# Kernel tuning notes

Measured on AMD Instinct MI355X. Metric: run time of the kernel, lower is better.

## Reference

```python
import jax, jax.numpy as jnp
import numpy as np

STATE_DIM = 128
FEATURES = 768
DT_MIN, DT_MAX = 0.001, 0.1


def setup_inputs() -> dict:
    key = jax.random.key(0)
    ks = jax.random.split(key, 8)
    B, S, F, N = 8, 4096, FEATURES, STATE_DIM
    n = jnp.arange(N, dtype=jnp.float32)
    # HiPPO-diag inits (deterministic)
    log_A_real = jnp.log(n + 0.5)
    A_imag = jnp.pi * n
    # lecun_normal: std = 1/sqrt(fan_in), fan_in = axis -2
    B_re = jax.random.normal(ks[0], (N, F), jnp.float32) / jnp.sqrt(N)
    B_im = jax.random.normal(ks[1], (N, F), jnp.float32) / jnp.sqrt(N)
    C_re = jax.random.normal(ks[2], (F, N), jnp.float32) / jnp.sqrt(F)
    C_im = jax.random.normal(ks[3], (F, N), jnp.float32) / jnp.sqrt(F)
    D = jax.random.normal(ks[4], (F,), jnp.float32)
    log_dt = jax.random.uniform(ks[5], (N,), jnp.float32,
                                minval=jnp.log(DT_MIN), maxval=jnp.log(DT_MAX))
    u = jax.random.normal(ks[6], (B, S, F), jnp.float32)
    return {"u": u, "log_A_real": log_A_real, "A_imag": A_imag,
            "B_re": B_re, "B_im": B_im, "C_re": C_re, "C_im": C_im,
            "D": D, "log_dt": log_dt}


def reference(u, log_A_real, A_imag, B_re, B_im, C_re, C_im, D, log_dt):
    B, S, F = u.shape
    N = log_A_real.shape[0]
    dt = jnp.exp(log_dt)                           # [N]
    A_diag = -jnp.exp(log_A_real) + 1j * A_imag    # [N] complex
    A_bar = jnp.exp(A_diag * dt)                   # [N] discretized A
    B_complex = B_re + 1j * B_im                   # [N, F]
    B_bar = (A_bar[:, None] - 1.0) / (A_diag[:, None] + 1e-08) * B_complex
    C_complex = C_re + 1j * C_im                   # [F, N]

    u_f = u.astype(jnp.float32)
    Bu = jnp.einsum('bsf,nf->bsn', u_f, B_bar)     # [B, S, N] complex
    A_exp = jnp.broadcast_to(A_bar[None, None, :], (B, S, N))

    def binary_operator(e1, e2):
        a1, b1 = e1
        a2, b2 = e2
        return (a1 * a2, a2 * b1 + b2)

    _, x_states = jax.lax.associative_scan(binary_operator, (A_exp, Bu), axis=1)
    y = jnp.einsum('fn,bsn->bsf', C_complex, x_states).real
    y = y + D[None, None, :] * u_f
    return y.astype(u.dtype)
```

## Files before the change

### kernel.cpp

```cpp
#include <hip/hip_runtime.h>
#include <hip/hip_bf16.h>
#include <math.h>

typedef __attribute__((ext_vector_type(8))) short short8;
typedef __attribute__((ext_vector_type(4))) float f32x4;
typedef __attribute__((ext_vector_type(4))) unsigned int uint4v;

constexpr int kF = 768;
constexpr int kN = 128;
constexpr int kB = 8;
constexpr int kS = 4096;
constexpr int kM = kB * kS;
constexpr int kChunks = 128;
constexpr int kClen = 32;

constexpr size_t kOffBw      = 4096;
constexpr size_t kOffCw      = 397312;
constexpr size_t kOffFinals  = 790528;
constexpr size_t kOffCarries = 1052672;
constexpr size_t kOffXbf     = 1314816;

__device__ __forceinline__ unsigned short f2bf(float f) {
    unsigned int u = __builtin_bit_cast(unsigned int, f);
    u += 0x7fffu + ((u >> 16) & 1u);
    return (unsigned short)(u >> 16);
}

#define LGKM0_BAR() do { \
    asm volatile("s_waitcnt lgkmcnt(0)" ::: "memory"); \
    __builtin_amdgcn_s_barrier(); \
    __builtin_amdgcn_sched_barrier(0); \
} while (0)

__global__ __launch_bounds__(128)
void pre1(const float* __restrict__ log_A_real, const float* __restrict__ A_imag,
          const float* __restrict__ log_dt, float* __restrict__ ws) {
    int n = threadIdx.x;
    float dt = expf(log_dt[n]);
    float ar = -expf(log_A_real[n]);
    float ai = A_imag[n];
    float er = expf(ar * dt);
    float Ar = er * cosf(ai * dt);
    float Ai = er * sinf(ai * dt);
    float dr = ar + 1e-8f, di = ai;
    float inv = 1.0f / (dr * dr + di * di);
    float nr = Ar - 1.0f, ni = Ai;
    float cr = (nr * dr + ni * di) * inv;
    float ci = (ni * dr - nr * di) * inv;
    float pr = 1.f, pi = 0.f;
    for (int i = 0; i < kClen; ++i) {
        float t = pr * Ar - pi * Ai;
        pi = pr * Ai + pi * Ar;
        pr = t;
    }
    ws[n] = Ar;        ws[128 + n] = Ai;
    ws[256 + n] = pr;  ws[384 + n] = pi;
    ws[512 + n] = cr;  ws[640 + n] = ci;
}

__global__ __launch_bounds__(256)
void pre2(const float* __restrict__ B_re, const float* __restrict__ B_im,
          const float* __restrict__ wsf, unsigned short* __restrict__ bw) {
    int id = blockIdx.x * 256 + threadIdx.x;
    int c = id / kF;
    int f = id - c * kF;
    int n = c & 127;
    float cr = wsf[512 + n], ci = wsf[640 + n];
    float br = B_re[n * kF + f], bi = B_im[n * kF + f];
    float v = (c < 128) ? (cr * br - ci * bi) : (cr * bi + ci * br);
    bw[id] = f2bf(v);
}

__global__ __launch_bounds__(256)
void pre3(const float* __restrict__ C_re, const float* __restrict__ C_im,
          unsigned short* __restrict__ cw) {
    int id = blockIdx.x * 256 + threadIdx.x;
    int f = id >> 8;
    int k = id & 255;
    float v = (k < 128) ? C_re[f * kN + k] : -C_im[f * kN + (k - 128)];
    cw[id] = f2bf(v);
}

__global__ __launch_bounds__(256, 2)
void gemm1(const float* __restrict__ A,
           const unsigned short* __restrict__ W,
           float* __restrict__ Cout) {
    constexpr int K = kF, KT = K / 32;
    __shared__ __align__(16) short As0[128 * 40];
    __shared__ __align__(16) short As1[128 * 40];
    __shared__ __align__(16) short Ws0[128 * 40];
    __shared__ __align__(16) short Ws1[128 * 40];

    const int gx = gridDim.x;
    const int nwg = gx * gridDim.y;
    const int orig = blockIdx.y * gx + blockIdx.x;
    const int cpx = nwg >> 3;
    const int sw = (orig & 7) * cpx + (orig >> 3);
    const int m0 = (sw / gx) * 128;
    const int n0 = (sw % gx) * 128;

    const int t = threadIdx.x;
    const int sr = t >> 1, sh = t & 1;

    const int wave = t >> 6, lane = t & 63;
    const int wr = wave >> 1, wc = wave & 1;
    const int lr = lane & 15, lg = lane >> 4;

    f32x4 acc[4][4] = {};

    f32x4 aA0, aA1, aA2, aA3, aB0, aB1, aB2, aB3;
    uint4v wA0, wA1, wB0, wB1;
    const float* aptr = A + (size_t)(m0 + sr) * K + sh * 16;
    const unsigned short* wptr = W + (size_t)(n0 + sr) * K + sh * 16;

#define G1_LOAD(SET, kt) do { \
    const float* p_ = aptr + (kt) * 32; \
    a##SET##0 = *(const f32x4*)p_;        a##SET##1 = *(const f32x4*)(p_ + 4); \
    a##SET##2 = *(const f32x4*)(p_ + 8);  a##SET##3 = *(const f32x4*)(p_ + 12); \
    const unsigned short* q_ = wptr + (kt) * 32; \
    w##SET##0 = *(const uint4v*)q_; w##SET##1 = *(const uint4v*)(q_ + 8); \
} while (0)

#define G1_WRITE(Asb, Wsb, a0, a1, a2, a3, w0, w1) do { \
    short h_[16]; \
    _Pragma("unroll") for (int e_ = 0; e_ < 4; ++e_) { \
        h_[e_]      = (short)f2bf(a0[e_]); \
        h_[4 + e_]  = (short)f2bf(a1[e_]); \
        h_[8 + e_]  = (short)f2bf(a2[e_]); \
        h_[12 + e_] = (short)f2bf(a3[e_]); \
    } \
    const int o_ = sr * 40 + sh * 16; \
    *(short8*)(&Asb[o_])     = *(short8*)&h_[0]; \
    *(short8*)(&Asb[o_ + 8]) = *(short8*)&h_[8]; \
    *(short8*)(&Wsb[o_])     = *(short8*)&w0; \
    *(short8*)(&Wsb[o_ + 8]) = *(short8*)&w1; \
} while (0)

#define G1_MMA(Asb, Wsb) do { \
    short8 ah_[4], bh_[4]; \
    _Pragma("unroll") for (int i_ = 0; i_ < 4; ++i_) { \
        ah_[i_] = *(const short8*)(&Asb[(wr * 64 + i_ * 16 + lr) * 40 + lg * 8]); \
        bh_[i_] = *(const short8*)(&Wsb[(wc * 64 + i_ * 16 + lr) * 40 + lg * 8]); \
    } \
    _Pragma("unroll") for (int i_ = 0; i_ < 4; ++i_) \
    _Pragma("unroll") for (int j_ = 0; j_ < 4; ++j_) \
        acc[i_][j_] = __builtin_amdgcn_mfma_f32_16x16x32_bf16(ah_[i_], bh_[j_], acc[i_][j_], 0, 0, 0); \
} while (0)

    G1_LOAD(A, 0);
    G1_LOAD(B, 1);
    for (int kt = 0; kt < KT; kt += 2) {
        G1_WRITE(As0, Ws0, aA0, aA1, aA2, aA3, wA0, wA1);
        if (kt + 2 < KT) G1_LOAD(A, kt + 2);
        LGKM0_BAR();
        G1_MMA(As0, Ws0);
        G1_WRITE(As1, Ws1, aB0, aB1, aB2, aB3, wB0, wB1);
        if (kt + 3 < KT) G1_LOAD(B, kt + 3);
        LGKM0_BAR();
        G1_MMA(As1, Ws1);
    }

#pragma unroll
    for (int i = 0; i < 4; ++i)
#pragma unroll
        for (int j = 0; j < 4; ++j) {
            const int col = n0 + wc * 64 + j * 16 + lr;
#pragma unroll
            for (int q = 0; q < 4; ++q) {
                const int row = m0 + wr * 64 + i * 16 + lg * 4 + q;
                Cout[(size_t)row * 256 + col] = acc[i][j][q];
            }
        }
#undef G1_LOAD
#undef G1_WRITE
#undef G1_MMA
}

__global__ __launch_bounds__(128)
void scanA(const float* __restrict__ Bu, const float* __restrict__ wsc,
           float* __restrict__ finals) {
    int n = threadIdx.x;
    int blk = blockIdx.x;
    int b = blk >> 7, c = blk & 127;
    float Ar = wsc[n], Ai = wsc[128 + n];
    float xr = 0.f, xi = 0.f;
    size_t base = ((size_t)(b * kS + c * kClen)) * 256;
#pragma unroll 8
    for (int s = 0; s < kClen; ++s) {
        float br = Bu[base + n], bi = Bu[base + 128 + n];
        float tr = Ar * xr - Ai * xi + br;
        xi = Ar * xi + Ai * xr + bi;
        xr = tr;
        base += 256;
    }
    finals[(size_t)blk * 256 + n] = xr;
    finals[(size_t)blk * 256 + 128 + n] = xi;
}

__global__ __launch_bounds__(128)
void scanB(const float* __restrict__ finals, const float* __restrict__ ws,
           float* __restrict__ carries) {
    int n = threadIdx.x;
    int b = blockIdx.x;
    float Pr = ws[256 + n], Pi = ws[384 + n];
    float xr = 0.f, xi = 0.f;
#pragma unroll 8
    for (int c = 0; c < kChunks; ++c) {
        size_t o = ((size_t)(b * kChunks + c)) * 256;
        carries[o + n] = xr;
        carries[o + 128 + n] = xi;
        float fr = finals[o + n], fi = finals[o + 128 + n];
        float tr = Pr * xr - Pi * xi + fr;
        xi = Pr * xi + Pi * xr + fi;
        xr = tr;
    }
}

__global__ __launch_bounds__(128)
void scanC(const float* __restrict__ Bu, const float* __restrict__ wsc,
           const float* __restrict__ carries, unsigned short* __restrict__ xbf) {
    int n = threadIdx.x;
    int blk = blockIdx.x;
    int b = blk >> 7, c = blk & 127;
    float Ar = wsc[n], Ai = wsc[128 + n];
    size_t co = (size_t)blk * 256;
    float xr = carries[co + n], xi = carries[co + 128 + n];
    size_t base = ((size_t)(b * kS + c * kClen)) * 256;
#pragma unroll 4
    for (int s = 0; s < kClen; ++s) {
        float br = Bu[base + n], bi = Bu[base + 128 + n];
        float tr = Ar * xr - Ai * xi + br;
        xi = Ar * xi + Ai * xr + bi;
        xr = tr;
        xbf[base + n]       = f2bf(xr);
        xbf[base + 128 + n] = f2bf(xi);
        base += 256;
    }
}

__global__ __launch_bounds__(256, 3)
void gemm2(const unsigned short* __restrict__ A,
           const unsigned short* __restrict__ W,
           float* __restrict__ Cout,
           const float* __restrict__ Dp, const float* __restrict__ Up) {
    constexpr int K = 256, KT = 8, Nc = kF;
    __shared__ __align__(16) short As0[128 * 40];
    __shared__ __align__(16) short As1[128 * 40];
    __shared__ __align__(16) short Ws0[128 * 40];
    __shared__ __align__(16) short Ws1[128 * 40];

    const int gx = gridDim.x;
    const int nwg = gx * gridDim.y;
    const int orig = blockIdx.y * gx + blockIdx.x;
    const int cpx = nwg >> 3;
    const int sw = (orig & 7) * cpx + (orig >> 3);
    const int m0 = (sw / gx) * 128;
    const int n0 = (sw % gx) * 128;

    const int t = threadIdx.x;
    const int sr = t >> 1, sh = t & 1;

    const int wave = t >> 6, lane = t & 63;
    const int wr = wave >> 1, wc = wave & 1;
    const int lr = lane & 15, lg = lane >> 4;

    f32x4 acc[4][4] = {};

    uint4v aA0, aA1, aB0, aB1;
    uint4v wA0, wA1, wB0, wB1;
    const unsigned short* aptr = A + (size_t)(m0 + sr) * K + sh * 16;
    const unsigned short* wptr = W + (size_t)(n0 + sr) * K + sh * 16;

#define G2_LOAD(SET, kt) do { \
    const unsigned short* p_ = aptr + (kt) * 32; \
    a##SET##0 = *(const uint4v*)p_; a##SET##1 = *(const uint4v*)(p_ + 8); \
    const unsigned short* q_ = wptr + (kt) * 32; \
    w##SET##0 = *(const uint4v*)q_; w##SET##1 = *(const uint4v*)(q_ + 8); \
} while (0)

#define G2_WRITE(Asb, Wsb, a0, a1, w0, w1) do { \
    const int o_ = sr * 40 + sh * 16; \
    *(short8*)(&Asb[o_])     = *(short8*)&a0; \
    *(short8*)(&Asb[o_ + 8]) = *(short8*)&a1; \
    *(short8*)(&Wsb[o_])     = *(short8*)&w0; \
    *(short8*)(&Wsb[o_ + 8]) = *(short8*)&w1; \
} while (0)

#define G2_MMA(Asb, Wsb) do { \
    short8 ah_[4], bh_[4]; \
    _Pragma("unroll") for (int i_ = 0; i_ < 4; ++i_) { \
        ah_[i_] = *(const short8*)(&Asb[(wr * 64 + i_ * 16 + lr) * 40 + lg * 8]); \
        bh_[i_] = *(const short8*)(&Wsb[(wc * 64 + i_ * 16 + lr) * 40 + lg * 8]); \
    } \
    _Pragma("unroll") for (int i_ = 0; i_ < 4; ++i_) \
    _Pragma("unroll") for (int j_ = 0; j_ < 4; ++j_) \
        acc[i_][j_] = __builtin_amdgcn_mfma_f32_16x16x32_bf16(ah_[i_], bh_[j_], acc[i_][j_], 0, 0, 0); \
} while (0)

    G2_LOAD(A, 0);
    G2_LOAD(B, 1);
    for (int kt = 0; kt < KT; kt += 2) {
        G2_WRITE(As0, Ws0, aA0, aA1, wA0, wA1);
        if (kt + 2 < KT) G2_LOAD(A, kt + 2);
        LGKM0_BAR();
        G2_MMA(As0, Ws0);
        G2_WRITE(As1, Ws1, aB0, aB1, wB0, wB1);
        if (kt + 3 < KT) G2_LOAD(B, kt + 3);
        LGKM0_BAR();
        G2_MMA(As1, Ws1);
    }

#pragma unroll
    for (int i = 0; i < 4; ++i)
#pragma unroll
        for (int j = 0; j < 4; ++j) {
            const int col = n0 + wc * 64 + j * 16 + lr;
#pragma unroll
            for (int q = 0; q < 4; ++q) {
                const int row = m0 + wr * 64 + i * 16 + lg * 4 + q;
                float v = acc[i][j][q];
                v = fmaf(Dp[col], Up[(size_t)row * Nc + col], v);
                Cout[(size_t)row * Nc + col] = v;
            }
        }
#undef G2_LOAD
#undef G2_WRITE
#undef G2_MMA
}

extern "C" void kernel_launch(void* const* d_in, const int* in_sizes, int n_in,
                              void* d_out, int out_size, void* d_ws, size_t ws_size,
                              hipStream_t stream) {
    const float* u          = (const float*)d_in[0];
    const float* log_A_real = (const float*)d_in[1];
    const float* A_imag     = (const float*)d_in[2];
    const float* B_re       = (const float*)d_in[3];
    const float* B_im       = (const float*)d_in[4];
    const float* C_re       = (const float*)d_in[5];
    const float* C_im       = (const float*)d_in[6];
    const float* D          = (const float*)d_in[7];
    const float* log_dt     = (const float*)d_in[8];

    char* wsb = (char*)d_ws;
    float* wsf            = (float*)wsb;
    unsigned short* bw    = (unsigned short*)(wsb + kOffBw);
    unsigned short* cw    = (unsigned short*)(wsb + kOffCw);
    float* finals         = (float*)(wsb + kOffFinals);
    float* carries        = (float*)(wsb + kOffCarries);
    unsigned short* xbf   = (unsigned short*)(wsb + kOffXbf);
    float* y              = (float*)d_out;
    float* Bu             = (float*)d_out;

    pre1<<<1, 128, 0, stream>>>(log_A_real, A_imag, log_dt, wsf);
    pre2<<<(256 * kF) / 256, 256, 0, stream>>>(B_re, B_im, wsf, bw);
    pre3<<<(kF * 256) / 256, 256, 0, stream>>>(C_re, C_im, cw);

    gemm1<<<dim3(2, kM / 128), 256, 0, stream>>>(u, bw, Bu);

    scanA<<<kB * kChunks, 128, 0, stream>>>(Bu, wsf, finals);
    scanB<<<kB, 128, 0, stream>>>(finals, wsf, carries);
    scanC<<<kB * kChunks, 128, 0, stream>>>(Bu, wsf, carries, xbf);

    gemm2<<<dim3(kF / 128, kM / 128), 256, 0, stream>>>(xbf, cw, y, D, u);
}
```

Before: 102.2 us.

## Shrink gemm1 M-tile to 64, triple-buffer register prefetch, raise occupancy

gemm1 now computes 64x128 output tiles instead of 128x128. This halves the per-thread accumulators and A staging registers and doubles the number of workgroups. Global loads move to a three-set register prefetch rotation, with a six-step unrolled loop over the 24 K-tiles. Launch bounds rise to 4 waves per SIMD for both gemm1 and gemm2, aiming at better latency hiding and more parallelism. The cost is lower data reuse per tile, so each W tile is loaded twice as often, and gemm2 may spill registers under the tighter bound.

Result: slower. 127.4 us (+24.6%).

```diff
diff --git a/kernel.cpp b/kernel.cpp
--- a/kernel.cpp
+++ b/kernel.cpp
@@ -81,13 +81,13 @@
     cw[id] = f2bf(v);
 }
 
-__global__ __launch_bounds__(256, 2)
+__global__ __launch_bounds__(256, 4)
 void gemm1(const float* __restrict__ A,
            const unsigned short* __restrict__ W,
            float* __restrict__ Cout) {
     constexpr int K = kF, KT = K / 32;
-    __shared__ __align__(16) short As0[128 * 40];
-    __shared__ __align__(16) short As1[128 * 40];
+    __shared__ __align__(16) short As0[64 * 40];
+    __shared__ __align__(16) short As1[64 * 40];
     __shared__ __align__(16) short Ws0[128 * 40];
     __shared__ __align__(16) short Ws1[128 * 40];
 
@@ -96,84 +96,89 @@
     const int orig = blockIdx.y * gx + blockIdx.x;
     const int cpx = nwg >> 3;
     const int sw = (orig & 7) * cpx + (orig >> 3);
-    const int m0 = (sw / gx) * 128;
+    const int m0 = (sw / gx) * 64;
     const int n0 = (sw % gx) * 128;
 
     const int t = threadIdx.x;
-    const int sr = t >> 1, sh = t & 1;
+    const int arow = t >> 2, aseg = t & 3;
+    const int wrow = t >> 1, wh = t & 1;
 
     const int wave = t >> 6, lane = t & 63;
     const int wr = wave >> 1, wc = wave & 1;
     const int lr = lane & 15, lg = lane >> 4;
 
-    f32x4 acc[4][4] = {};
-
-    f32x4 aA0, aA1, aA2, aA3, aB0, aB1, aB2, aB3;
-    uint4v wA0, wA1, wB0, wB1;
-    const float* aptr = A + (size_t)(m0 + sr) * K + sh * 16;
-    const unsigned short* wptr = W + (size_t)(n0 + sr) * K + sh * 16;
+    f32x4 acc[2][4] = {};
+
+    f32x4 aA0, aA1, aB0, aB1, aC0, aC1;
+    uint4v wA0, wA1, wB0, wB1, wC0, wC1;
+    const float* aptr = A + (size_t)(m0 + arow) * K + aseg * 8;
+    const unsigned short* wptr = W + (size_t)(n0 + wrow) * K + wh * 16;
 
 #define G1_LOAD(SET, kt) do { \
     const float* p_ = aptr + (kt) * 32; \
-    a##SET##0 = *(const f32x4*)p_;        a##SET##1 = *(const f32x4*)(p_ + 4); \
-    a##SET##2 = *(const f32x4*)(p_ + 8);  a##SET##3 = *(const f32x4*)(p_ + 12); \
+    a##SET##0 = *(const f32x4*)p_; a##SET##1 = *(const f32x4*)(p_ + 4); \
     const unsigned short* q_ = wptr + (kt) * 32; \
     w##SET##0 = *(const uint4v*)q_; w##SET##1 = *(const uint4v*)(q_ + 8); \
 } while (0)
 
-#define G1_WRITE(Asb, Wsb, a0, a1, a2, a3, w0, w1) do { \
-    short h_[16]; \
+#define G1_WRITE(Asb, Wsb, SET) do { \
+    short h_[8]; \
     _Pragma("unroll") for (int e_ = 0; e_ < 4; ++e_) { \
-        h_[e_]      = (short)f2bf(a0[e_]); \
-        h_[4 + e_]  = (short)f2bf(a1[e_]); \
-        h_[8 + e_]  = (short)f2bf(a2[e_]); \
-        h_[12 + e_] = (short)f2bf(a3[e_]); \
+        h_[e_]     = (short)f2bf(a##SET##0[e_]); \
+        h_[4 + e_] = (short)f2bf(a##SET##1[e_]); \
     } \
-    const int o_ = sr * 40 + sh * 16; \
-    *(short8*)(&Asb[o_])     = *(short8*)&h_[0]; \
-    *(short8*)(&Asb[o_ + 8]) = *(short8*)&h_[8]; \
-    *(short8*)(&Wsb[o_])     = *(short8*)&w0; \
-    *(short8*)(&Wsb[o_ + 8]) = *(short8*)&w1; \
+    *(short8*)(&Asb[arow * 40 + aseg * 8]) = *(short8*)h_; \
+    const int o_ = wrow * 40 + wh * 16; \
+    *(short8*)(&Wsb[o_])     = *(short8*)&w##SET##0; \
+    *(short8*)(&Wsb[o_ + 8]) = *(short8*)&w##SET##1; \
 } while (0)
 
 #define G1_MMA(Asb, Wsb) do { \
-    short8 ah_[4], bh_[4]; \
-    _Pragma("unroll") for (int i_ = 0; i_ < 4; ++i_) { \
-        ah_[i_] = *(const short8*)(&Asb[(wr * 64 + i_ * 16 + lr) * 40 + lg * 8]); \
-        bh_[i_] = *(const short8*)(&Wsb[(wc * 64 + i_ * 16 + lr) * 40 + lg * 8]); \
-    } \
-    _Pragma("unroll") for (int i_ = 0; i_ < 4; ++i_) \
+    short8 ah_[2], bh_[4]; \
+    _Pragma("unroll") for (int i_ = 0; i_ < 2; ++i_) \
+        ah_[i_] = *(const short8*)(&Asb[(wr * 32 + i_ * 16 + lr) * 40 + lg * 8]); \
+    _Pragma("unroll") for (int j_ = 0; j_ < 4; ++j_) \
+        bh_[j_] = *(const short8*)(&Wsb[(wc * 64 + j_ * 16 + lr) * 40 + lg * 8]); \
+    _Pragma("unroll") for (int i_ = 0; i_ < 2; ++i_) \
     _Pragma("unroll") for (int j_ = 0; j_ < 4; ++j_) \
         acc[i_][j_] = __builtin_amdgcn_mfma_f32_16x16x32_bf16(ah_[i_], bh_[j_], acc[i_][j_], 0, 0, 0); \
 } while (0)
 
+#define G1_STEP(Asb, Wsb, SET, ktn) do { \
+    G1_WRITE(Asb, Wsb, SET); \
+    if ((ktn) < KT) G1_LOAD(SET, ktn); \
+    LGKM0_BAR(); \
+    G1_MMA(Asb, Wsb); \
+} while (0)
+
     G1_LOAD(A, 0);
     G1_LOAD(B, 1);
-    for (int kt = 0; kt < KT; kt += 2) {
-        G1_WRITE(As0, Ws0, aA0, aA1, aA2, aA3, wA0, wA1);
-        if (kt + 2 < KT) G1_LOAD(A, kt + 2);
-        LGKM0_BAR();
-        G1_MMA(As0, Ws0);
-        G1_WRITE(As1, Ws1, aB0, aB1, aB2, aB3, wB0, wB1);
-        if (kt + 3 < KT) G1_LOAD(B, kt + 3);
-        LGKM0_BAR();
-        G1_MMA(As1, Ws1);
-    }
-
-#pragma unroll
-    for (int i = 0; i < 4; ++i)
+    G1_LOAD(C, 2);
+    for (int it = 0; it < 4; ++it) {
+        const int kt = it * 6;
+        G1_STEP(As0, Ws0, A, kt + 3);
+        G1_STEP(As1, Ws1, B, kt + 4);
+        G1_STEP(As0, Ws0, C, kt + 5);
+        G1_STEP(As1, Ws1, A, kt + 6);
+        G1_STEP(As0, Ws0, B, kt + 7);
+        G1_STEP(As1, Ws1, C, kt + 8);
+    }
+
+#pragma unroll
+    for (int i = 0; i < 2; ++i)
 #pragma unroll
         for (int j = 0; j < 4; ++j) {
             const int col = n0 + wc * 64 + j * 16 + lr;
 #pragma unroll
             for (int q = 0; q < 4; ++q) {
-                const int row = m0 + wr * 64 + i * 16 + lg * 4 + q;
+                const int row = m0 + wr * 32 + i * 16 + lg * 4 + q;
                 Cout[(size_t)row * 256 + col] = acc[i][j][q];
             }
         }
 #undef G1_LOAD
 #undef G1_WRITE
 #undef G1_MMA
+#undef G1_STEP
 }
 
 __global__ __launch_bounds__(128)
@@ -238,7 +243,7 @@
     }
 }
 
-__global__ __launch_bounds__(256, 3)
+__global__ __launch_bounds__(256, 4)
 void gemm2(const unsigned short* __restrict__ A,
            const unsigned short* __restrict__ W,
            float* __restrict__ Cout,
@@ -355,7 +360,7 @@
     pre2<<<(256 * kF) / 256, 256, 0, stream>>>(B_re, B_im, wsf, bw);
     pre3<<<(kF * 256) / 256, 256, 0, stream>>>(C_re, C_im, cw);
 
-    gemm1<<<dim3(2, kM / 128), 256, 0, stream>>>(u, bw, Bu);
+    gemm1<<<dim3(2, kM / 64), 256, 0, stream>>>(u, bw, Bu);
 
     scanA<<<kB * kChunks, 128, 0, stream>>>(Bu, wsf, finals);
     scanB<<<kB, 128, 0, stream>>>(finals, wsf, carries);
```

## Use direct global-to-LDS loads with triple-buffered XOR-swizzled tiles in gemm1

Applied to the files above, without the earlier changes.

Replaces the register-staged double-buffered gemm1 mainloop with global_load_lds direct copies into a three-slot LDS ring, using vmcnt waits so loads run two tiles ahead. A is now stored as fp32 in LDS and converted to bf16 at fragment-read time, and both tiles use an XOR swizzle to avoid bank conflicts. The aim is to cut register pressure and VALU work on the load path and to overlap memory with MFMA. The cost is more LDS (72KB per block, which may lower occupancy from two blocks per CU) and the bf16 conversions are repeated on LDS reads.

After: 101.9 us. About the same (-0.3%).

```diff
diff --git a/kernel.cpp b/kernel.cpp
--- a/kernel.cpp
+++ b/kernel.cpp
@@ -24,6 +24,12 @@
     unsigned int u = __builtin_bit_cast(unsigned int, f);
     u += 0x7fffu + ((u >> 16) & 1u);
     return (unsigned short)(u >> 16);
+}
+
+__device__ __forceinline__ void gload16(const void* g, void* l) {
+    __builtin_amdgcn_global_load_lds(
+        (const __attribute__((address_space(1))) void*)g,
+        (__attribute__((address_space(3))) void*)l, 16, 0, 0);
 }
 
 #define LGKM0_BAR() do { \
@@ -86,10 +92,8 @@
            const unsigned short* __restrict__ W,
            float* __restrict__ Cout) {
     constexpr int K = kF, KT = K / 32;
-    __shared__ __align__(16) short As0[128 * 40];
-    __shared__ __align__(16) short As1[128 * 40];
-    __shared__ __align__(16) short Ws0[128 * 40];
-    __shared__ __align__(16) short Ws1[128 * 40];
+    constexpr int SLOT = 24576;
+    __shared__ __align__(16) char smem[3 * SLOT];
 
     const int gx = gridDim.x;
     const int nwg = gx * gridDim.y;
@@ -100,64 +104,71 @@
     const int n0 = (sw % gx) * 128;
 
     const int t = threadIdx.x;
-    const int sr = t >> 1, sh = t & 1;
-
     const int wave = t >> 6, lane = t & 63;
     const int wr = wave >> 1, wc = wave & 1;
     const int lr = lane & 15, lg = lane >> 4;
+    const int l3 = lane >> 3, l7 = lane & 7;
+    const int uswz = l7 ^ l3;
+
+    const float* aBase = A + (size_t)(m0 + wave * 32 + l3) * K + uswz * 4;
+    const unsigned short* wBase =
+        W + (size_t)(n0 + wave * 32 + l3 * 2 + (uswz >> 2)) * K + (uswz & 3) * 8;
 
     f32x4 acc[4][4] = {};
 
-    f32x4 aA0, aA1, aA2, aA3, aB0, aB1, aB2, aB3;
-    uint4v wA0, wA1, wB0, wB1;
-    const float* aptr = A + (size_t)(m0 + sr) * K + sh * 16;
-    const unsigned short* wptr = W + (size_t)(n0 + sr) * K + sh * 16;
-
-#define G1_LOAD(SET, kt) do { \
-    const float* p_ = aptr + (kt) * 32; \
-    a##SET##0 = *(const f32x4*)p_;        a##SET##1 = *(const f32x4*)(p_ + 4); \
-    a##SET##2 = *(const f32x4*)(p_ + 8);  a##SET##3 = *(const f32x4*)(p_ + 12); \
-    const unsigned short* q_ = wptr + (kt) * 32; \
-    w##SET##0 = *(const uint4v*)q_; w##SET##1 = *(const uint4v*)(q_ + 8); \
-} while (0)
-
-#define G1_WRITE(Asb, Wsb, a0, a1, a2, a3, w0, w1) do { \
-    short h_[16]; \
-    _Pragma("unroll") for (int e_ = 0; e_ < 4; ++e_) { \
-        h_[e_]      = (short)f2bf(a0[e_]); \
-        h_[4 + e_]  = (short)f2bf(a1[e_]); \
-        h_[8 + e_]  = (short)f2bf(a2[e_]); \
-        h_[12 + e_] = (short)f2bf(a3[e_]); \
-    } \
-    const int o_ = sr * 40 + sh * 16; \
-    *(short8*)(&Asb[o_])     = *(short8*)&h_[0]; \
-    *(short8*)(&Asb[o_ + 8]) = *(short8*)&h_[8]; \
-    *(short8*)(&Wsb[o_])     = *(short8*)&w0; \
-    *(short8*)(&Wsb[o_ + 8]) = *(short8*)&w1; \
-} while (0)
-
-#define G1_MMA(Asb, Wsb) do { \
+#define G1_ISSUE(kt_, slotbase_) do { \
+    const float* aT_ = aBase + (size_t)(kt_) * 32; \
+    const unsigned short* wT_ = wBase + (size_t)(kt_) * 32; \
+    char* sA_ = (slotbase_); \
+    char* sW_ = (slotbase_) + 16384; \
+    _Pragma("unroll") for (int c_ = 0; c_ < 4; ++c_) \
+        gload16(aT_ + c_ * 8 * K, sA_ + (wave * 4 + c_) * 1024); \
+    _Pragma("unroll") for (int c_ = 0; c_ < 2; ++c_) \
+        gload16(wT_ + c_ * 16 * K, sW_ + (wave * 2 + c_) * 1024); \
+} while (0)
+
+#define G1_MMA_SLOT(slotbase_) do { \
+    const char* sA_ = (slotbase_); \
+    const char* sW_ = (slotbase_) + 16384; \
     short8 ah_[4], bh_[4]; \
     _Pragma("unroll") for (int i_ = 0; i_ < 4; ++i_) { \
-        ah_[i_] = *(const short8*)(&Asb[(wr * 64 + i_ * 16 + lr) * 40 + lg * 8]); \
-        bh_[i_] = *(const short8*)(&Wsb[(wc * 64 + i_ * 16 + lr) * 40 + lg * 8]); \
+        const int row_ = wr * 64 + i_ * 16 + lr; \
+        const f32x4 fL_ = *(const f32x4*)(sA_ + row_ * 128 + (((lg * 2)     ^ (lr & 7)) * 16)); \
+        const f32x4 fH_ = *(const f32x4*)(sA_ + row_ * 128 + (((lg * 2 + 1) ^ (lr & 7)) * 16)); \
+        short8 v_; \
+        _Pragma("unroll") for (int e_ = 0; e_ < 4; ++e_) { \
+            v_[e_]     = (short)f2bf(fL_[e_]); \
+            v_[4 + e_] = (short)f2bf(fH_[e_]); \
+        } \
+        ah_[i_] = v_; \
+    } \
+    _Pragma("unroll") for (int j_ = 0; j_ < 4; ++j_) { \
+        const int row_ = wc * 64 + j_ * 16 + lr; \
+        const int d_ = row_ >> 1; \
+        const int u_ = (((lr & 1) * 4 + lg) ^ (d_ & 7)) * 16; \
+        bh_[j_] = *(const short8*)(sW_ + d_ * 128 + u_); \
     } \
     _Pragma("unroll") for (int i_ = 0; i_ < 4; ++i_) \
     _Pragma("unroll") for (int j_ = 0; j_ < 4; ++j_) \
         acc[i_][j_] = __builtin_amdgcn_mfma_f32_16x16x32_bf16(ah_[i_], bh_[j_], acc[i_][j_], 0, 0, 0); \
 } while (0)
 
-    G1_LOAD(A, 0);
-    G1_LOAD(B, 1);
-    for (int kt = 0; kt < KT; kt += 2) {
-        G1_WRITE(As0, Ws0, aA0, aA1, aA2, aA3, wA0, wA1);
-        if (kt + 2 < KT) G1_LOAD(A, kt + 2);
-        LGKM0_BAR();
-        G1_MMA(As0, Ws0);
-        G1_WRITE(As1, Ws1, aB0, aB1, aB2, aB3, wB0, wB1);
-        if (kt + 3 < KT) G1_LOAD(B, kt + 3);
-        LGKM0_BAR();
-        G1_MMA(As1, Ws1);
+    G1_ISSUE(0, smem);
+    G1_ISSUE(1, smem + SLOT);
+
+    int slot = 0;
+    for (int kt = 0; kt < KT; ++kt) {
+        if (kt < KT - 1) { asm volatile("s_waitcnt vmcnt(6)" ::: "memory"); }
+        else             { asm volatile("s_waitcnt vmcnt(0)" ::: "memory"); }
+        __builtin_amdgcn_s_barrier();
+        __builtin_amdgcn_sched_barrier(0);
+        char* sb = smem + slot * SLOT;
+        if (kt + 2 < KT) {
+            char* nb = smem + (slot == 0 ? 2 * SLOT : (slot - 1) * SLOT);
+            G1_ISSUE(kt + 2, nb);
+        }
+        G1_MMA_SLOT(sb);
+        slot = (slot == 2) ? 0 : slot + 1;
     }
 
 #pragma unroll
@@ -171,9 +182,8 @@
                 Cout[(size_t)row * 256 + col] = acc[i][j][q];
             }
         }
-#undef G1_LOAD
-#undef G1_WRITE
-#undef G1_MMA
+#undef G1_ISSUE
+#undef G1_MMA_SLOT
 }
 
 __global__ __launch_bounds__(128)
```

## Load gemm1 MFMA operands directly from global memory, dropping LDS staging

Applied to the files above, without the earlier changes.

The first projection GEMM no longer stages the fp32 input and bf16 weight tiles through double-buffered shared memory. Each lane now loads its MFMA fragments straight from global memory, converting to bf16 in registers, and relies on L1/L2 for reuse across waves. This removes the LDS writes, reads and barriers. In exchange it adds redundant global loads, since two waves read the same A rows and two read the same W rows, and it loses the explicit software prefetch overlap.

After: 144.5 us. 41.3% more time.

```diff
diff --git a/kernel.cpp b/kernel.cpp
--- a/kernel.cpp
+++ b/kernel.cpp
@@ -86,10 +86,6 @@
            const unsigned short* __restrict__ W,
            float* __restrict__ Cout) {
     constexpr int K = kF, KT = K / 32;
-    __shared__ __align__(16) short As0[128 * 40];
-    __shared__ __align__(16) short As1[128 * 40];
-    __shared__ __align__(16) short Ws0[128 * 40];
-    __shared__ __align__(16) short Ws1[128 * 40];
 
     const int gx = gridDim.x;
     const int nwg = gx * gridDim.y;
@@ -100,64 +96,40 @@
     const int n0 = (sw % gx) * 128;
 
     const int t = threadIdx.x;
-    const int sr = t >> 1, sh = t & 1;
-
     const int wave = t >> 6, lane = t & 63;
     const int wr = wave >> 1, wc = wave & 1;
     const int lr = lane & 15, lg = lane >> 4;
 
     f32x4 acc[4][4] = {};
 
-    f32x4 aA0, aA1, aA2, aA3, aB0, aB1, aB2, aB3;
-    uint4v wA0, wA1, wB0, wB1;
-    const float* aptr = A + (size_t)(m0 + sr) * K + sh * 16;
-    const unsigned short* wptr = W + (size_t)(n0 + sr) * K + sh * 16;
-
-#define G1_LOAD(SET, kt) do { \
-    const float* p_ = aptr + (kt) * 32; \
-    a##SET##0 = *(const f32x4*)p_;        a##SET##1 = *(const f32x4*)(p_ + 4); \
-    a##SET##2 = *(const f32x4*)(p_ + 8);  a##SET##3 = *(const f32x4*)(p_ + 12); \
-    const unsigned short* q_ = wptr + (kt) * 32; \
-    w##SET##0 = *(const uint4v*)q_; w##SET##1 = *(const uint4v*)(q_ + 8); \
-} while (0)
-
-#define G1_WRITE(Asb, Wsb, a0, a1, a2, a3, w0, w1) do { \
-    short h_[16]; \
-    _Pragma("unroll") for (int e_ = 0; e_ < 4; ++e_) { \
-        h_[e_]      = (short)f2bf(a0[e_]); \
-        h_[4 + e_]  = (short)f2bf(a1[e_]); \
-        h_[8 + e_]  = (short)f2bf(a2[e_]); \
-        h_[12 + e_] = (short)f2bf(a3[e_]); \
-    } \
-    const int o_ = sr * 40 + sh * 16; \
-    *(short8*)(&Asb[o_])     = *(short8*)&h_[0]; \
-    *(short8*)(&Asb[o_ + 8]) = *(short8*)&h_[8]; \
-    *(short8*)(&Wsb[o_])     = *(short8*)&w0; \
-    *(short8*)(&Wsb[o_ + 8]) = *(short8*)&w1; \
-} while (0)
-
-#define G1_MMA(Asb, Wsb) do { \
-    short8 ah_[4], bh_[4]; \
-    _Pragma("unroll") for (int i_ = 0; i_ < 4; ++i_) { \
-        ah_[i_] = *(const short8*)(&Asb[(wr * 64 + i_ * 16 + lr) * 40 + lg * 8]); \
-        bh_[i_] = *(const short8*)(&Wsb[(wc * 64 + i_ * 16 + lr) * 40 + lg * 8]); \
-    } \
-    _Pragma("unroll") for (int i_ = 0; i_ < 4; ++i_) \
-    _Pragma("unroll") for (int j_ = 0; j_ < 4; ++j_) \
-        acc[i_][j_] = __builtin_amdgcn_mfma_f32_16x16x32_bf16(ah_[i_], bh_[j_], acc[i_][j_], 0, 0, 0); \
-} while (0)
-
-    G1_LOAD(A, 0);
-    G1_LOAD(B, 1);
-    for (int kt = 0; kt < KT; kt += 2) {
-        G1_WRITE(As0, Ws0, aA0, aA1, aA2, aA3, wA0, wA1);
-        if (kt + 2 < KT) G1_LOAD(A, kt + 2);
-        LGKM0_BAR();
-        G1_MMA(As0, Ws0);
-        G1_WRITE(As1, Ws1, aB0, aB1, aB2, aB3, wB0, wB1);
-        if (kt + 3 < KT) G1_LOAD(B, kt + 3);
-        LGKM0_BAR();
-        G1_MMA(As1, Ws1);
+    const float* aBase = A + (size_t)(m0 + wr * 64 + lr) * K + lg * 8;
+    const unsigned short* wBase = W + (size_t)(n0 + wc * 64 + lr) * K + lg * 8;
+
+#pragma unroll 2
+    for (int kt = 0; kt < KT; ++kt) {
+        const int k0 = kt * 32;
+        short8 ah[4], bh[4];
+#pragma unroll
+        for (int i = 0; i < 4; ++i) {
+            const float* p = aBase + (size_t)i * 16 * K + k0;
+            const f32x4 lo = *(const f32x4*)p;
+            const f32x4 hi = *(const f32x4*)(p + 4);
+            short8 v;
+#pragma unroll
+            for (int e = 0; e < 4; ++e) {
+                v[e]     = (short)f2bf(lo[e]);
+                v[4 + e] = (short)f2bf(hi[e]);
+            }
+            ah[i] = v;
+        }
+#pragma unroll
+        for (int j = 0; j < 4; ++j)
+            bh[j] = *(const short8*)(wBase + (size_t)j * 16 * K + k0);
+#pragma unroll
+        for (int i = 0; i < 4; ++i)
+#pragma unroll
+            for (int j = 0; j < 4; ++j)
+                acc[i][j] = __builtin_amdgcn_mfma_f32_16x16x32_bf16(ah[i], bh[j], acc[i][j], 0, 0, 0);
     }
 
 #pragma unroll
@@ -171,9 +143,6 @@
                 Cout[(size_t)row * 256 + col] = acc[i][j][q];
             }
         }
-#undef G1_LOAD
-#undef G1_WRITE
-#undef G1_MMA
 }
 
 __global__ __launch_bounds__(128)
```
